# Kernel optimization log

Measured on AMD Instinct MI355X. Metric: run time of the kernel, lower is better.

Reference implementation:

```python
import jax, jax.numpy as jnp
import numpy as np

B, C, H = 2, 256, 64
INTER = 64


def setup_inputs() -> dict:
    key = jax.random.key(0)
    ks = jax.random.split(key, 10)
    scale = 1.0 / np.sqrt(C)
    x = jax.random.normal(ks[0], (B, C, H, H), dtype=jnp.float32)
    # binary hole mask (1 = foreground/hole region)
    mask = jnp.round(jax.random.uniform(ks[1], (B, 1, H, H), dtype=jnp.float32))
    def w(k, shape, s):
        return jax.random.normal(k, shape, dtype=jnp.float32) * s
    return {
        "x": x,
        "mask": mask,
        "w_theta_s": w(ks[2], (INTER, C), scale),
        "w_phi_s": w(ks[3], (INTER, C), scale),
        "w_gate_s": w(ks[4], (INTER, C), scale),
        "w_theta_c": w(ks[5], (INTER, C), scale),
        "w_phi_c": w(ks[6], (INTER, C), scale),
        "w_gate_c": w(ks[7], (INTER, C), scale),
        "w_out": w(ks[8], (C, INTER), 1.0 / np.sqrt(INTER)),
    }


def _nonlocal_branch(q_src, kv_src, w_theta, w_phi, w_gate):
    # q_src, kv_src: [B, C, N]; weights: [inter, C]
    K = jnp.einsum('oc,bcn->bon', w_theta, kv_src)   # [B, inter, N]
    Q = jnp.einsum('oc,bcn->bon', w_phi, q_src)      # [B, inter, N]
    score = jnp.einsum('bom,bon->bmn', Q, K)         # [B, Nq, Nk]
    score = jax.nn.softmax(score, axis=-1)
    V = jnp.einsum('oc,bcn->bon', w_gate, kv_src)    # [B, inter, N]
    feat = jnp.einsum('bon,bmn->bom', V, score)      # [B, inter, Nq]
    return feat, score


def reference(x, mask, w_theta_s, w_phi_s, w_gate_s,
              w_theta_c, w_phi_c, w_gate_c, w_out):
    b, c, h = x.shape[0], x.shape[1], x.shape[2]
    n = h * h
    fg = (x * mask).reshape(b, c, n)          # foreground tokens
    bg = (x * (1.0 - mask)).reshape(b, c, n)  # background tokens
    feat_self, score_self = _nonlocal_branch(fg, fg, w_theta_s, w_phi_s, w_gate_s)
    feat_cross, score_cross = _nonlocal_branch(fg, bg, w_theta_c, w_phi_c, w_gate_c)
    fused = jnp.einsum('co,bon->bcn', w_out, feat_self + feat_cross)
    feat = x + fused.reshape(b, c, h, h)
    return feat, score_self, score_cross
```

## Files before the change

### kernel.cpp

```cpp
#include <hip/hip_runtime.h>
#include <hip/hip_bf16.h>
#include <stdint.h>

#define NBATCH 2
#define NCH    256
#define NTOK   4096
#define NINT   64
#define CHW    64
#define QCOLS  1024
#define NCHQ   (QCOLS/CHW)

typedef float  f32x4  __attribute__((ext_vector_type(4)));
typedef __bf16 bf16x8 __attribute__((ext_vector_type(8)));
union U16x8 { uint4 u; bf16x8 b; };

#define SZBF      ((size_t)NTOK*NINT)
#define BF_TOTAL  ((size_t)NBATCH*10*SZBF*2)
#define FEAT_OFF  (BF_TOTAL)
#define RL_OFF_B  ((size_t)4194304)

#define OUT_SELF  ((size_t)2097152)
#define OUT_CROSS ((size_t)35651584)
#define FPART_OFF_F (OUT_SELF)
#define LPART_OFF_F (OUT_SELF + (size_t)4194304)

__device__ inline unsigned short f2bf(float x){
  unsigned int u = __builtin_bit_cast(unsigned int, x);
  u = (u + 0x7FFFu + ((u>>16)&1u)) >> 16;
  return (unsigned short)u;
}
__device__ inline float bf2f(unsigned short s){
  unsigned int u = ((unsigned int)s)<<16;
  return __builtin_bit_cast(float, u);
}

typedef __attribute__((address_space(3))) unsigned int lds_u32_t;
typedef __attribute__((address_space(1))) const unsigned int gbl_u32_t;
__device__ inline void async16(const void* g, void* l){
  __builtin_amdgcn_global_load_lds((gbl_u32_t*)g, (lds_u32_t*)l, 16, 0, 0);
}

__global__ __launch_bounds__(256) void k_proj(
    const float* __restrict__ x, const float* __restrict__ mask,
    const float* __restrict__ wts, const float* __restrict__ wps,
    const float* __restrict__ wgs, const float* __restrict__ wtc,
    const float* __restrict__ wpc, const float* __restrict__ wgc,
    char* __restrict__ ws)
{
  int nt = blockIdx.x;
  int j  = blockIdx.y;
  int b  = blockIdx.z;
  const float* W; int isBg, mode, arrH, arrL;
  switch (j) {
    case 0: W=wts; isBg=0; mode=0; arrH=2; arrL=3; break;
    case 1: W=wps; isBg=0; mode=0; arrH=0; arrL=1; break;
    case 2: W=wgs; isBg=0; mode=1; arrH=8; arrL=8; break;
    case 3: W=wpc; isBg=0; mode=0; arrH=4; arrL=5; break;
    case 4: W=wtc; isBg=1; mode=0; arrH=6; arrL=7; break;
    default:W=wgc; isBg=1; mode=1; arrH=9; arrL=9; break;
  }
  __shared__ float xm[256*64];
  __shared__ float msk[64];
  int t = threadIdx.x;
  if (t < 64) {
    float m = mask[(size_t)b*NTOK + nt*64 + t];
    msk[t] = isBg ? (1.0f - m) : m;
  }
  __syncthreads();
  const float* xb = x + (size_t)b*NCH*NTOK + nt*64;
  for (int it = 0; it < 64; ++it) {
    int flat = it*256 + t; int c = flat>>6, nl = flat&63;
    xm[flat] = xb[(size_t)c*NTOK + nl] * msk[nl];
  }
  __syncthreads();
  int nl = t & 63;
  int o0 = __builtin_amdgcn_readfirstlane((t>>6)*16);
  const float* Wr = W + (size_t)o0*256;
  float acc[16];
  #pragma unroll
  for (int i=0;i<16;i++) acc[i]=0.0f;
  #pragma unroll 4
  for (int c=0;c<256;c++){
    float xv = xm[c*64+nl];
    #pragma unroll
    for (int i=0;i<16;i++) acc[i] += Wr[i*256 + c] * xv;
  }
  int n = nt*64 + nl;
  if (mode==0){
    unsigned short* Ah = (unsigned short*)ws + ((size_t)b*10 + arrH)*SZBF;
    unsigned short* Al = (unsigned short*)ws + ((size_t)b*10 + arrL)*SZBF;
    #pragma unroll
    for (int i=0;i<16;i++){
      float v = acc[i];
      unsigned short h = f2bf(v);
      float r = v - bf2f(h);
      Ah[(size_t)n*NINT + o0+i] = h;
      Al[(size_t)n*NINT + o0+i] = f2bf(r);
    }
  } else {
    unsigned short* V = (unsigned short*)ws + ((size_t)b*10 + arrH)*SZBF;
    #pragma unroll
    for (int i=0;i<16;i++) V[(size_t)(o0+i)*NTOK + n] = f2bf(acc[i]);
  }
}

__global__ __launch_bounds__(256) void k_s1(char* __restrict__ ws, float* __restrict__ out)
{
  __shared__ __align__(16) char smem[41984];

  int blk = blockIdx.x;
  int xcd = blk & 7, idx = blk >> 3;
  int bbr = xcd >> 1;
  int unit = ((xcd & 1) << 7) | idx;
  int qtr = unit & 3, mb = unit >> 2;
  int b = bbr >> 1, br = bbr & 1;
  const unsigned short* Qh = (const unsigned short*)ws + ((size_t)b*10 + (br?4:0))*SZBF;
  const unsigned short* Ql = Qh + SZBF;
  const unsigned short* Kh = (const unsigned short*)ws + ((size_t)b*10 + (br?6:2))*SZBF;
  const unsigned short* Kl = Kh + SZBF;
  const unsigned short* Vv = (const unsigned short*)ws + ((size_t)b*10 + (br?9:8))*SZBF;

  int t = threadIdx.x, lane = t&63, w = t>>6;
  int rowb = lane&15, q4 = lane>>4, ko = q4*8;
  int m0 = mb*64 + w*16, mrow = m0 + rowb;

  unsigned short* lPw = (unsigned short*)(smem + 32768 + w*2304);

  U16x8 qh[2], ql[2];
  #pragma unroll
  for (int kk=0;kk<2;kk++){
    qh[kk].u = *(const uint4*)(Qh + (size_t)mrow*NINT + kk*32 + ko);
    ql[kk].u = *(const uint4*)(Ql + (size_t)mrow*NINT + kk*32 + ko);
  }

  auto lkbase = [&](int buf)->unsigned short*{
    return (unsigned short*)(smem + (size_t)buf*16384);
  };
  auto stage = [&](int ch, int buf){
    int n0 = qtr*QCOLS + ch*CHW;
    const unsigned short* gH = Kh + (size_t)n0*NINT;
    const unsigned short* gL = Kl + (size_t)n0*NINT;
    unsigned short* LB = lkbase(buf);
    #pragma unroll
    for (int it=0; it<2; ++it){
      int f = it*256 + t;
      int r = f>>3, g = f&7, gs = g ^ (r&7);
      size_t goff = (size_t)r*64 + gs*8;
      async16(gH + goff, LB + (size_t)f*8);
      async16(gL + goff, LB + 4096 + (size_t)f*8);
    }
  };

  f32x4 fac[4];
  #pragma unroll
  for (int ot=0;ot<4;ot++) fac[ot] = (f32x4){0.0f,0.0f,0.0f,0.0f};
  float Lacc = 0.0f;

  stage(0, 0);
  for (int ch=0; ch<NCHQ; ++ch){
    int cur = ch & 1;
    asm volatile("s_waitcnt vmcnt(0)" ::: "memory");
    __syncthreads();
    if (ch+1 < NCHQ) stage(ch+1, cur^1);
    unsigned short* LB = lkbase(cur);
    int n0 = qtr*QCOLS + ch*CHW;
    #pragma unroll
    for (int t8=0; t8<4; ++t8){
      int row = t8*16 + rowb;
      f32x4 s = {0.0f,0.0f,0.0f,0.0f};
      #pragma unroll
      for (int kk=0; kk<2; ++kk){
        int soff = row*64 + (((kk*4 + q4) ^ (row&7))*8);
        U16x8 ah, al;
        ah.u = *(const uint4*)(LB + soff);
        al.u = *(const uint4*)(LB + 4096 + soff);
        s = __builtin_amdgcn_mfma_f32_16x16x32_bf16(ah.b, qh[kk].b, s, 0,0,0);
        s = __builtin_amdgcn_mfma_f32_16x16x32_bf16(ah.b, ql[kk].b, s, 0,0,0);
        s = __builtin_amdgcn_mfma_f32_16x16x32_bf16(al.b, qh[kk].b, s, 0,0,0);
      }
      float p0=__expf(s[0]), p1=__expf(s[1]), p2=__expf(s[2]), p3=__expf(s[3]);
      Lacc += (p0+p1)+(p2+p3);
      unsigned int lo = (unsigned int)f2bf(p0) | ((unsigned int)f2bf(p1)<<16);
      unsigned int hi = (unsigned int)f2bf(p2) | ((unsigned int)f2bf(p3)<<16);
      uint2 pk; pk.x = lo; pk.y = hi;
      *(uint2*)(lPw + rowb*72 + t8*16 + q4*4) = pk;
    }
    asm volatile("s_waitcnt lgkmcnt(0)" ::: "memory");
    #pragma unroll
    for (int kk4=0; kk4<2; ++kk4){
      U16x8 pa;
      pa.u = *(const uint4*)(lPw + rowb*72 + kk4*32 + ko);
      #pragma unroll
      for (int ot=0; ot<4; ++ot){
        U16x8 vb;
        vb.u = *(const uint4*)(Vv + (size_t)(ot*16+rowb)*NTOK + n0 + kk4*32 + ko);
        fac[ot] = __builtin_amdgcn_mfma_f32_16x16x32_bf16(pa.b, vb.b, fac[ot], 0,0,0);
      }
    }
    asm volatile("s_waitcnt lgkmcnt(0)" ::: "memory");
  }

  #pragma unroll
  for (int d=16; d<64; d<<=1) Lacc += __shfl_xor(Lacc, d, 64);
  if (q4==0)
    out[LPART_OFF_F + (size_t)(bbr*4+qtr)*NTOK + m0 + rowb] = Lacc;

  float* FP = out + FPART_OFF_F + (size_t)(bbr*4+qtr)*NTOK*NINT;
  #pragma unroll
  for (int ot=0; ot<4; ++ot)
    #pragma unroll
    for (int r=0; r<4; ++r)
      FP[(size_t)(m0 + q4*4 + r)*NINT + ot*16 + rowb] = fac[ot][r];
}

__global__ __launch_bounds__(256) void k_comb(char* __restrict__ ws, float* __restrict__ out)
{
  int blk = blockIdx.x;
  int bbr = blk >> 6, mb = blk & 63;
  const float* FP = out + FPART_OFF_F;
  const float* LP = out + LPART_OFF_F;
  float* feat = (float*)(ws + FEAT_OFF) + (size_t)bbr*NTOK*NINT;
  float* rL = (float*)(ws + RL_OFF_B) + (size_t)bbr*NTOK;
  int t = threadIdx.x;
  __shared__ float rls[64];
  if (t < 64) {
    int row = mb*64 + t;
    float L = 0.0f;
    #pragma unroll
    for (int q=0;q<4;q++) L += LP[(size_t)(bbr*4+q)*NTOK + row];
    float r = 1.0f / L;
    rls[t] = r;
    rL[row] = r;
  }
  __syncthreads();
  int o = t & 63, rg = t >> 6;
  for (int it=0; it<16; ++it){
    int rloc = it*4 + rg, row = mb*64 + rloc;
    float s = 0.0f;
    #pragma unroll
    for (int q=0;q<4;q++)
      s += FP[((size_t)(bbr*4+q)*NTOK + row)*NINT + o];
    feat[(size_t)row*NINT + o] = s * rls[rloc];
  }
}

__global__ __launch_bounds__(256) void k_s2(const char* __restrict__ ws, float* __restrict__ out)
{
  __shared__ __align__(16) char smem[32768];

  int blk = blockIdx.x;
  int xcd = blk & 7, idx = blk >> 3;
  int bbr = xcd >> 1;
  int unit = ((xcd & 1) << 7) | idx;
  int qtr = unit & 3, mb = unit >> 2;
  int b = bbr >> 1, br = bbr & 1;
  const unsigned short* Qh = (const unsigned short*)ws + ((size_t)b*10 + (br?4:0))*SZBF;
  const unsigned short* Ql = Qh + SZBF;
  const unsigned short* Kh = (const unsigned short*)ws + ((size_t)b*10 + (br?6:2))*SZBF;
  const unsigned short* Kl = Kh + SZBF;

  int t = threadIdx.x, lane = t&63, w = t>>6;
  int rowb = lane&15, q4 = lane>>4, ko = q4*8;
  int m0 = mb*64 + w*16, mrow = m0 + rowb;

  float rLp = ((const float*)(ws + RL_OFF_B))[(size_t)bbr*NTOK + mrow];

  U16x8 qh[2], ql[2];
  #pragma unroll
  for (int kk=0;kk<2;kk++){
    qh[kk].u = *(const uint4*)(Qh + (size_t)mrow*NINT + kk*32 + ko);
    ql[kk].u = *(const uint4*)(Ql + (size_t)mrow*NINT + kk*32 + ko);
  }

  auto lkbase = [&](int buf)->unsigned short*{
    return (unsigned short*)(smem + (size_t)buf*16384);
  };
  auto stage = [&](int ch, int buf){
    int n0 = qtr*QCOLS + ch*CHW;
    const unsigned short* gH = Kh + (size_t)n0*NINT;
    const unsigned short* gL = Kl + (size_t)n0*NINT;
    unsigned short* LB = lkbase(buf);
    #pragma unroll
    for (int it=0; it<2; ++it){
      int f = it*256 + t;
      int r = f>>3, g = f&7, gs = g ^ (r&7);
      size_t goff = (size_t)r*64 + gs*8;
      async16(gH + goff, LB + (size_t)f*8);
      async16(gL + goff, LB + 4096 + (size_t)f*8);
    }
  };

  float* outS = out + (br ? OUT_CROSS : OUT_SELF) + (size_t)b*NTOK*NTOK;

  stage(0, 0);
  for (int ch=0; ch<NCHQ; ++ch){
    int cur = ch & 1;
    if (ch == 0) { asm volatile("s_waitcnt vmcnt(0)" ::: "memory"); }
    else         { asm volatile("s_waitcnt vmcnt(4)" ::: "memory"); }
    __syncthreads();
    if (ch+1 < NCHQ) stage(ch+1, cur^1);
    __builtin_amdgcn_sched_barrier(0);
    unsigned short* LB = lkbase(cur);
    int n0 = qtr*QCOLS + ch*CHW;
    #pragma unroll
    for (int t8=0; t8<4; ++t8){
      int row = t8*16 + rowb;
      f32x4 s = {0.0f,0.0f,0.0f,0.0f};
      #pragma unroll
      for (int kk=0; kk<2; ++kk){
        int soff = row*64 + (((kk*4 + q4) ^ (row&7))*8);
        U16x8 ah, al;
        ah.u = *(const uint4*)(LB + soff);
        al.u = *(const uint4*)(LB + 4096 + soff);
        s = __builtin_amdgcn_mfma_f32_16x16x32_bf16(ah.b, qh[kk].b, s, 0,0,0);
        s = __builtin_amdgcn_mfma_f32_16x16x32_bf16(ah.b, ql[kk].b, s, 0,0,0);
        s = __builtin_amdgcn_mfma_f32_16x16x32_bf16(al.b, qh[kk].b, s, 0,0,0);
      }
      f32x4 p;
      p[0] = __expf(s[0])*rLp; p[1] = __expf(s[1])*rLp;
      p[2] = __expf(s[2])*rLp; p[3] = __expf(s[3])*rLp;
      __builtin_nontemporal_store(p,
          (f32x4*)(outS + (size_t)mrow*NTOK + n0 + t8*16 + q4*4));
    }
  }
}

__global__ __launch_bounds__(256) void k_epi(
    const float* __restrict__ x, const float* __restrict__ wout,
    const char* __restrict__ ws, float* __restrict__ out)
{
  int nt = blockIdx.x, b = blockIdx.y;
  int t = threadIdx.x, nl = t&63;
  const float* feat = (const float*)(ws + FEAT_OFF);
  __shared__ float fs[64][65];
  for (int it=0; it<16; ++it){
    int flat = it*256 + t; int n_l = flat>>6, o = flat&63;
    size_t r0 = ((size_t)(b*2+0)*NTOK + nt*64 + n_l)*NINT + o;
    size_t r1 = ((size_t)(b*2+1)*NTOK + nt*64 + n_l)*NINT + o;
    fs[n_l][o] = feat[r0] + feat[r1];
  }
  __syncthreads();
  float f[64];
  #pragma unroll
  for (int o=0;o<64;o++) f[o] = fs[nl][o];
  int c0 = __builtin_amdgcn_readfirstlane((t>>6)*64);
  const float* wr = wout + (size_t)c0*64;
  for (int cc=0; cc<64; ++cc){
    int c = c0 + cc;
    float acc = x[((size_t)b*NCH + c)*NTOK + nt*64 + nl];
    #pragma unroll
    for (int o=0;o<64;o++) acc += wr[cc*64+o]*f[o];
    out[((size_t)b*NCH + c)*NTOK + nt*64 + nl] = acc;
  }
}

extern "C" void kernel_launch(void* const* d_in, const int* in_sizes, int n_in,
                              void* d_out, int out_size, void* d_ws, size_t ws_size,
                              hipStream_t stream)
{
  const float* x    = (const float*)d_in[0];
  const float* mask = (const float*)d_in[1];
  const float* wts  = (const float*)d_in[2];
  const float* wps  = (const float*)d_in[3];
  const float* wgs  = (const float*)d_in[4];
  const float* wtc  = (const float*)d_in[5];
  const float* wpc  = (const float*)d_in[6];
  const float* wgc  = (const float*)d_in[7];
  const float* wout = (const float*)d_in[8];
  float* out = (float*)d_out;
  char*  ws  = (char*)d_ws;
  (void)in_sizes; (void)n_in; (void)out_size; (void)ws_size;

  k_proj <<<dim3(64,6,NBATCH), 256, 0, stream>>>(x, mask, wts, wps, wgs, wtc, wpc, wgc, ws);
  k_s1   <<<dim3(1024), 256, 0, stream>>>(ws, out);
  k_comb <<<dim3(256),  256, 0, stream>>>(ws, out);
  k_s2   <<<dim3(1024), 256, 0, stream>>>(ws, out);
  k_epi  <<<dim3(64,NBATCH), 256, 0, stream>>>(x, wout, ws, out);
}
```

Baseline: 583.8 us.

## Fuse partial-combine into epilogue, swizzle P tile in LDS, use raw barriers

The combine kernel is split in two. A tiny kernel now computes only the reciprocal softmax denominators, and the epilogue sums the four quarter partials, scales them and adds the two branches directly. This removes the intermediate feat buffer round trip. The epilogue now runs before the score-writing kernel, because the partials live in the score output region that kernel overwrites. In k_s1 the per-wave P staging tile drops its padding for an XOR swizzle to avoid LDS bank conflicts with less shared memory. __syncthreads is replaced by a bare s_barrier with scheduling barriers, which risks subtle ordering issues around async LDS loads.

```diff
diff --git a/kernel.cpp b/kernel.cpp
--- a/kernel.cpp
+++ b/kernel.cpp
@@ -15,8 +15,6 @@
 union U16x8 { uint4 u; bf16x8 b; };
 
 #define SZBF      ((size_t)NTOK*NINT)
-#define BF_TOTAL  ((size_t)NBATCH*10*SZBF*2)
-#define FEAT_OFF  (BF_TOTAL)
 #define RL_OFF_B  ((size_t)4194304)
 
 #define OUT_SELF  ((size_t)2097152)
@@ -38,6 +36,11 @@
 typedef __attribute__((address_space(1))) const unsigned int gbl_u32_t;
 __device__ inline void async16(const void* g, void* l){
   __builtin_amdgcn_global_load_lds((gbl_u32_t*)g, (lds_u32_t*)l, 16, 0, 0);
+}
+__device__ inline void wgbar(){
+  asm volatile("" ::: "memory");
+  __builtin_amdgcn_s_barrier();
+  asm volatile("" ::: "memory");
 }
 
 __global__ __launch_bounds__(256) void k_proj(
@@ -106,7 +109,7 @@
 
 __global__ __launch_bounds__(256) void k_s1(char* __restrict__ ws, float* __restrict__ out)
 {
-  __shared__ __align__(16) char smem[41984];
+  __shared__ __align__(16) char smem[40960];
 
   int blk = blockIdx.x;
   int xcd = blk & 7, idx = blk >> 3;
@@ -124,7 +127,7 @@
   int rowb = lane&15, q4 = lane>>4, ko = q4*8;
   int m0 = mb*64 + w*16, mrow = m0 + rowb;
 
-  unsigned short* lPw = (unsigned short*)(smem + 32768 + w*2304);
+  unsigned short* lPw = (unsigned short*)(smem + 32768 + w*2048);
 
   U16x8 qh[2], ql[2];
   #pragma unroll
@@ -160,8 +163,10 @@
   for (int ch=0; ch<NCHQ; ++ch){
     int cur = ch & 1;
     asm volatile("s_waitcnt vmcnt(0)" ::: "memory");
-    __syncthreads();
+    wgbar();
     if (ch+1 < NCHQ) stage(ch+1, cur^1);
+    asm volatile("" ::: "memory");
+    __builtin_amdgcn_sched_barrier(0);
     unsigned short* LB = lkbase(cur);
     int n0 = qtr*QCOLS + ch*CHW;
     #pragma unroll
@@ -183,13 +188,17 @@
       unsigned int lo = (unsigned int)f2bf(p0) | ((unsigned int)f2bf(p1)<<16);
       unsigned int hi = (unsigned int)f2bf(p2) | ((unsigned int)f2bf(p3)<<16);
       uint2 pk; pk.x = lo; pk.y = hi;
-      *(uint2*)(lPw + rowb*72 + t8*16 + q4*4) = pk;
+      int g  = t8*2 + (q4>>1);
+      int gs = g ^ (rowb&7);
+      *(uint2*)(lPw + rowb*64 + gs*8 + (q4&1)*4) = pk;
     }
     asm volatile("s_waitcnt lgkmcnt(0)" ::: "memory");
+    __builtin_amdgcn_sched_barrier(0);
     #pragma unroll
     for (int kk4=0; kk4<2; ++kk4){
+      int rs = (kk4*4 + q4) ^ (rowb&7);
       U16x8 pa;
-      pa.u = *(const uint4*)(lPw + rowb*72 + kk4*32 + ko);
+      pa.u = *(const uint4*)(lPw + rowb*64 + rs*8);
       #pragma unroll
       for (int ot=0; ot<4; ++ot){
         U16x8 vb;
@@ -213,34 +222,50 @@
       FP[(size_t)(m0 + q4*4 + r)*NINT + ot*16 + rowb] = fac[ot][r];
 }
 
-__global__ __launch_bounds__(256) void k_comb(char* __restrict__ ws, float* __restrict__ out)
-{
-  int blk = blockIdx.x;
-  int bbr = blk >> 6, mb = blk & 63;
+__global__ __launch_bounds__(256) void k_rl(char* __restrict__ ws, const float* __restrict__ out)
+{
+  int idxg = blockIdx.x*256 + threadIdx.x;
+  int bbr = idxg >> 12, row = idxg & 4095;
+  const float* LP = out + LPART_OFF_F;
+  float L = 0.0f;
+  #pragma unroll
+  for (int q=0;q<4;q++) L += LP[(size_t)(bbr*4+q)*NTOK + row];
+  ((float*)(ws + RL_OFF_B))[(size_t)bbr*NTOK + row] = 1.0f / L;
+}
+
+__global__ __launch_bounds__(256) void k_epi(
+    const float* __restrict__ x, const float* __restrict__ wout,
+    const char* __restrict__ ws, float* __restrict__ out)
+{
+  int nt = blockIdx.x, b = blockIdx.y;
+  int t = threadIdx.x, nl = t&63;
   const float* FP = out + FPART_OFF_F;
-  const float* LP = out + LPART_OFF_F;
-  float* feat = (float*)(ws + FEAT_OFF) + (size_t)bbr*NTOK*NINT;
-  float* rL = (float*)(ws + RL_OFF_B) + (size_t)bbr*NTOK;
-  int t = threadIdx.x;
-  __shared__ float rls[64];
-  if (t < 64) {
-    int row = mb*64 + t;
-    float L = 0.0f;
-    #pragma unroll
-    for (int q=0;q<4;q++) L += LP[(size_t)(bbr*4+q)*NTOK + row];
-    float r = 1.0f / L;
-    rls[t] = r;
-    rL[row] = r;
+  const float* rL = (const float*)(ws + RL_OFF_B);
+  __shared__ float fs[64][65];
+  int b0 = b*2, b1 = b*2+1;
+  for (int it=0; it<16; ++it){
+    int flat = it*256 + t; int n_l = flat>>6, o = flat&63;
+    int row = nt*64 + n_l;
+    float s0=0.0f, s1=0.0f;
+    #pragma unroll
+    for (int q=0;q<4;q++){
+      s0 += FP[((size_t)(b0*4+q)*NTOK + row)*NINT + o];
+      s1 += FP[((size_t)(b1*4+q)*NTOK + row)*NINT + o];
+    }
+    fs[n_l][o] = s0*rL[(size_t)b0*NTOK+row] + s1*rL[(size_t)b1*NTOK+row];
   }
   __syncthreads();
-  int o = t & 63, rg = t >> 6;
-  for (int it=0; it<16; ++it){
-    int rloc = it*4 + rg, row = mb*64 + rloc;
-    float s = 0.0f;
-    #pragma unroll
-    for (int q=0;q<4;q++)
-      s += FP[((size_t)(bbr*4+q)*NTOK + row)*NINT + o];
-    feat[(size_t)row*NINT + o] = s * rls[rloc];
+  float f[64];
+  #pragma unroll
+  for (int o=0;o<64;o++) f[o] = fs[nl][o];
+  int c0 = __builtin_amdgcn_readfirstlane((t>>6)*64);
+  const float* wr = wout + (size_t)c0*64;
+  for (int cc=0; cc<64; ++cc){
+    int c = c0 + cc;
+    float acc = x[((size_t)b*NCH + c)*NTOK + nt*64 + nl];
+    #pragma unroll
+    for (int o=0;o<64;o++) acc += wr[cc*64+o]*f[o];
+    out[((size_t)b*NCH + c)*NTOK + nt*64 + nl] = acc;
   }
 }
 
@@ -297,8 +322,9 @@
     int cur = ch & 1;
     if (ch == 0) { asm volatile("s_waitcnt vmcnt(0)" ::: "memory"); }
     else         { asm volatile("s_waitcnt vmcnt(4)" ::: "memory"); }
-    __syncthreads();
+    wgbar();
     if (ch+1 < NCHQ) stage(ch+1, cur^1);
+    asm volatile("" ::: "memory");
     __builtin_amdgcn_sched_barrier(0);
     unsigned short* LB = lkbase(cur);
     int n0 = qtr*QCOLS + ch*CHW;
@@ -325,35 +351,6 @@
   }
 }
 
-__global__ __launch_bounds__(256) void k_epi(
-    const float* __restrict__ x, const float* __restrict__ wout,
-    const char* __restrict__ ws, float* __restrict__ out)
-{
-  int nt = blockIdx.x, b = blockIdx.y;
-  int t = threadIdx.x, nl = t&63;
-  const float* feat = (const float*)(ws + FEAT_OFF);
-  __shared__ float fs[64][65];
-  for (int it=0; it<16; ++it){
-    int flat = it*256 + t; int n_l = flat>>6, o = flat&63;
-    size_t r0 = ((size_t)(b*2+0)*NTOK + nt*64 + n_l)*NINT + o;
-    size_t r1 = ((size_t)(b*2+1)*NTOK + nt*64 + n_l)*NINT + o;
-    fs[n_l][o] = feat[r0] + feat[r1];
-  }
-  __syncthreads();
-  float f[64];
-  #pragma unroll
-  for (int o=0;o<64;o++) f[o] = fs[nl][o];
-  int c0 = __builtin_amdgcn_readfirstlane((t>>6)*64);
-  const float* wr = wout + (size_t)c0*64;
-  for (int cc=0; cc<64; ++cc){
-    int c = c0 + cc;
-    float acc = x[((size_t)b*NCH + c)*NTOK + nt*64 + nl];
-    #pragma unroll
-    for (int o=0;o<64;o++) acc += wr[cc*64+o]*f[o];
-    out[((size_t)b*NCH + c)*NTOK + nt*64 + nl] = acc;
-  }
-}
-
 extern "C" void kernel_launch(void* const* d_in, const int* in_sizes, int n_in,
                               void* d_out, int out_size, void* d_ws, size_t ws_size,
                               hipStream_t stream)
@@ -373,7 +370,7 @@
 
   k_proj <<<dim3(64,6,NBATCH), 256, 0, stream>>>(x, mask, wts, wps, wgs, wtc, wpc, wgc, ws);
   k_s1   <<<dim3(1024), 256, 0, stream>>>(ws, out);
-  k_comb <<<dim3(256),  256, 0, stream>>>(ws, out);
+  k_rl   <<<dim3(64),   256, 0, stream>>>(ws, out);
+  k_epi  <<<dim3(64,NBATCH), 256, 0, stream>>>(x, wout, ws, out);
   k_s2   <<<dim3(1024), 256, 0, stream>>>(ws, out);
-  k_epi  <<<dim3(64,NBATCH), 256, 0, stream>>>(x, wout, ws, out);
-}
+}
```

Result: faster. 555.6 us (-4.8%).
